# Performance work log

Measured on AMD Instinct MI355X. Metric: run time of the kernel, lower is better.

The kernel has to match this reference:

```python
import jax, jax.numpy as jnp
import numpy as np

EPS_NORM = 1e-12   # F.normalize eps
EPS_SCALE = 1e-5   # activation scale clamp


def _weight_quant(w):
    # ternary (sign) quantization with mean-abs scale
    scale = jnp.mean(jnp.abs(w))
    u = jnp.sign(w - jnp.mean(w))
    return u, scale


def _activation_quant(x):
    # SimpleRMSNorm: l2-normalize over last dim, times dim**-0.5
    dim_scale = x.shape[-1] ** -0.5
    l2 = jnp.linalg.norm(x, axis=-1, keepdims=True)
    xn = x / jnp.maximum(l2, EPS_NORM) * dim_scale
    # per-token int8 scale
    scale = 127.0 / jnp.maximum(jnp.max(jnp.abs(xn), axis=-1, keepdims=True), EPS_SCALE)
    y = jnp.clip(jnp.round(xn * scale), -128.0, 127.0)
    return y, scale


def setup_inputs() -> dict:
    key = jax.random.key(0)
    kx, kw, kb = jax.random.split(key, 3)
    B, S, D, O = 4, 8192, 1024, 1024
    x = jax.random.normal(kx, (B, S, D), dtype=jnp.float32)
    w = jax.random.normal(kw, (O, D), dtype=jnp.float32)
    b = jax.random.normal(kb, (O,), dtype=jnp.float32)
    return {"x": x, "w": w, "b": b}


def reference(x, w, b):
    w_q, w_scale = _weight_quant(w)          # [O,D], scalar
    b_q, b_scale = _weight_quant(b)          # [O], scalar
    x_q, x_scale = _activation_quant(x)      # [B,S,D], [B,S,1]
    # mm + broadcast bias add, then dequant by product of all three scales
    y = jnp.einsum('bsd,od->bso', x_q, w_q) + b_q
    return y / (w_scale * x_scale * b_scale)
```

## Files before the change

### kernel.cpp

```cpp
#include <hip/hip_runtime.h>
#include <cstdint>
#include <cstddef>


typedef __attribute__((ext_vector_type(4))) int int4v;

static constexpr int DIM = 1024;
static constexpr int OUTF = 1024;
static constexpr int MROWS = 32768;
static constexpr float INV_WN = 1.0f / (1024.0f * 1024.0f);
static constexpr float INV_BN = 1.0f / 1024.0f;

#define OFF_XSCALE 1024
#define OFF_WQ 132096
#define OFF_XQ 1180672

__device__ inline float wave_sum(float v) {
#pragma unroll
  for (int off = 32; off; off >>= 1) v += __shfl_xor(v, off);
  return v;
}
__device__ inline float wave_max(float v) {
#pragma unroll
  for (int off = 32; off; off >>= 1) v = fmaxf(v, __shfl_xor(v, off));
  return v;
}

__global__ __launch_bounds__(256) void reduce_wb(const float* __restrict__ w,
                                                 const float* __restrict__ b,
                                                 float* __restrict__ red) {
  __shared__ float ss[4], sa[4];
  const int t = threadIdx.x;
  const int lane = t & 63, wv = t >> 6;
  float s = 0.0f, a = 0.0f;
  const float4* w4 = (const float4*)w;
  const int idx = blockIdx.x * 256 + t;
#pragma unroll
  for (int i = 0; i < 4; ++i) {
    float4 v = w4[idx + i * 65536];
    s += (v.x + v.y) + (v.z + v.w);
    a += (fabsf(v.x) + fabsf(v.y)) + (fabsf(v.z) + fabsf(v.w));
  }
  s = wave_sum(s);
  a = wave_sum(a);
  if (lane == 0) { ss[wv] = s; sa[wv] = a; }
  __syncthreads();
  if (t == 0) atomicAdd(&red[0], (ss[0] + ss[1]) + (ss[2] + ss[3]));
  if (t == 1) atomicAdd(&red[1], (sa[0] + sa[1]) + (sa[2] + sa[3]));
  if (blockIdx.x == 0) {
    __syncthreads();
    float4 v = ((const float4*)b)[t];
    float s2 = (v.x + v.y) + (v.z + v.w);
    float a2 = (fabsf(v.x) + fabsf(v.y)) + (fabsf(v.z) + fabsf(v.w));
    s2 = wave_sum(s2);
    a2 = wave_max(a2) * 0.0f + wave_sum(a2);
    if (lane == 0) { ss[wv] = s2; sa[wv] = a2; }
    __syncthreads();
    if (t == 0) {
      red[2] = (ss[0] + ss[1]) + (ss[2] + ss[3]);
      red[3] = (sa[0] + sa[1]) + (sa[2] + sa[3]);
    }
  }
}

__global__ __launch_bounds__(256) void quant_w(const float* __restrict__ w,
                                               const float* __restrict__ red,
                                               signed char* __restrict__ wq) {
  const float wmean = red[0] * INV_WN;
  const int idx = blockIdx.x * 256 + threadIdx.x;
  float4 v = ((const float4*)w)[idx];
  int q0, q1, q2, q3;
  float d;
  d = v.x - wmean; q0 = d > 0.f ? 1 : (d < 0.f ? -1 : 0);
  d = v.y - wmean; q1 = d > 0.f ? 1 : (d < 0.f ? -1 : 0);
  d = v.z - wmean; q2 = d > 0.f ? 1 : (d < 0.f ? -1 : 0);
  d = v.w - wmean; q3 = d > 0.f ? 1 : (d < 0.f ? -1 : 0);
  const int pk = (q0 & 0xff) | ((q1 & 0xff) << 8) | ((q2 & 0xff) << 16) | ((q3 & 0xff) << 24);
  ((int*)wq)[idx] = pk;
}

__global__ __launch_bounds__(256) void quant_x(const float* __restrict__ x,
                                               signed char* __restrict__ xq,
                                               float* __restrict__ xscale) {
  const int wv = threadIdx.x >> 6;
  const int lane = threadIdx.x & 63;
  const int row = blockIdx.x * 4 + wv;
  const float4* xr = (const float4*)(x + (size_t)row * DIM);
  float4 v[4];
  float ss = 0.0f, ma = 0.0f;
#pragma unroll
  for (int it = 0; it < 4; ++it) {
    v[it] = xr[it * 64 + lane];
    ss += v[it].x * v[it].x + v[it].y * v[it].y + v[it].z * v[it].z + v[it].w * v[it].w;
    ma = fmaxf(ma, fmaxf(fmaxf(fabsf(v[it].x), fabsf(v[it].y)),
                         fmaxf(fabsf(v[it].z), fabsf(v[it].w))));
  }
  ss = wave_sum(ss);
  ma = wave_max(ma);

  const float l2 = sqrtf(ss);
  const float inv = 0.03125f / fmaxf(l2, 1e-12f);
  const float scale = 127.0f / fmaxf(ma * inv, 1e-5f);
  const float f = inv * scale;

  int* outp = (int*)(xq + (size_t)row * DIM);
#pragma unroll
  for (int it = 0; it < 4; ++it) {
    const int q0 = (int)fminf(fmaxf(rintf(v[it].x * f), -128.f), 127.f);
    const int q1 = (int)fminf(fmaxf(rintf(v[it].y * f), -128.f), 127.f);
    const int q2 = (int)fminf(fmaxf(rintf(v[it].z * f), -128.f), 127.f);
    const int q3 = (int)fminf(fmaxf(rintf(v[it].w * f), -128.f), 127.f);
    outp[it * 64 + lane] =
        (q0 & 0xff) | ((q1 & 0xff) << 8) | ((q2 & 0xff) << 16) | ((q3 & 0xff) << 24);
  }
  if (lane == 0) xscale[row] = scale;
}

#define BM 128
#define BN 128
#define BKB 128

__global__ __launch_bounds__(256) void gemm_i8(
    const signed char* __restrict__ Aq,
    const signed char* __restrict__ Wq,
    const float* __restrict__ bias,
    const float* __restrict__ red,
    const float* __restrict__ xscale,
    float* __restrict__ out) {
  __shared__ signed char As[BM * BKB];
  __shared__ signed char Bs[BN * BKB];

  const int t = threadIdx.x;
  const int lane = t & 63;
  const int wv = t >> 6;
  const int quad = lane >> 4;
  const int r16 = lane & 15;
  const int wm = (wv >> 1) * 64;
  const int wn = (wv & 1) * 64;
  const int bm = blockIdx.y;
  const int bn = blockIdx.x;

  int4v acc[4][4] = {};

  const char* Ab = (const char*)(Aq + (size_t)bm * BM * DIM);
  const char* Bb = (const char*)(Wq + (size_t)bn * BN * DIM);

  const int srow = lane >> 3;
  const int sbyte = (lane & 7) * 16;

  for (int k0 = 0; k0 < DIM; k0 += BKB) {
#pragma unroll
    for (int i = 0; i < 4; ++i) {
      const int c = wv * 4 + i;
      const int row = c * 8 + srow;
      __builtin_amdgcn_global_load_lds(
          (const __attribute__((address_space(1))) void*)(Ab + (size_t)row * DIM + k0 + sbyte),
          (__attribute__((address_space(3))) void*)((char*)As + c * 1024 + lane * 16),
          16, 0, 0);
      __builtin_amdgcn_global_load_lds(
          (const __attribute__((address_space(1))) void*)(Bb + (size_t)row * DIM + k0 + sbyte),
          (__attribute__((address_space(3))) void*)((char*)Bs + c * 1024 + lane * 16),
          16, 0, 0);
    }
    __syncthreads();
#pragma unroll
    for (int s = 0; s < 2; ++s) {
      int4v af[4], bf[4];
#pragma unroll
      for (int i = 0; i < 4; ++i) {
        af[i] = *(const int4v*)(As + (wm + i * 16 + r16) * BKB + s * 64 + quad * 16);
        bf[i] = *(const int4v*)(Bs + (wn + i * 16 + r16) * BKB + s * 64 + quad * 16);
      }
#pragma unroll
      for (int i = 0; i < 4; ++i)
#pragma unroll
        for (int j = 0; j < 4; ++j)
          acc[i][j] = __builtin_amdgcn_mfma_i32_16x16x64_i8(af[i], bf[j], acc[i][j], 0, 0, 0);
    }
    __syncthreads();
  }

  const float wscale = red[1] * INV_WN;
  const float bscale = red[3] * INV_BN;
  const float bmean = red[2] * INV_BN;
  const float wb = wscale * bscale;

  float rec[4][4];
#pragma unroll
  for (int i = 0; i < 4; ++i)
#pragma unroll
    for (int rr = 0; rr < 4; ++rr) {
      const int m = bm * BM + wm + i * 16 + quad * 4 + rr;
      rec[i][rr] = 1.0f / (wb * xscale[m]);
    }

#pragma unroll
  for (int j = 0; j < 4; ++j) {
    const int n = bn * BN + wn + j * 16 + r16;
    const float bd = bias[n] - bmean;
    const int bq = bd > 0.f ? 1 : (bd < 0.f ? -1 : 0);
#pragma unroll
    for (int i = 0; i < 4; ++i) {
      const int mg = bm * BM + wm + i * 16 + quad * 4;
      float* po = out + (size_t)mg * OUTF + n;
#pragma unroll
      for (int rr = 0; rr < 4; ++rr)
        po[(size_t)rr * OUTF] = (float)(acc[i][j][rr] + bq) * rec[i][rr];
    }
  }
}

extern "C" void kernel_launch(void* const* d_in, const int* in_sizes, int n_in,
                              void* d_out, int out_size, void* d_ws, size_t ws_size,
                              hipStream_t stream) {
  const float* x = (const float*)d_in[0];
  const float* w = (const float*)d_in[1];
  const float* b = (const float*)d_in[2];
  float* out = (float*)d_out;
  char* ws = (char*)d_ws;

  float* red = (float*)ws;
  float* xscale = (float*)(ws + OFF_XSCALE);
  signed char* wq = (signed char*)(ws + OFF_WQ);
  signed char* xq = (signed char*)(ws + OFF_XQ);

  hipMemsetAsync(red, 0, 4 * sizeof(float), stream);
  reduce_wb<<<256, 256, 0, stream>>>(w, b, red);
  quant_w<<<1024, 256, 0, stream>>>(w, red, wq);
  quant_x<<<MROWS / 4, 256, 0, stream>>>(x, xq, xscale);
  gemm_i8<<<dim3(OUTF / BN, MROWS / BM), 256, 0, stream>>>(xq, wq, b, red, xscale, out);
}
```

Before: 296.7 us.

## Fuse activation quantization into GEMM with full-K LDS-resident A tile

```diff
diff --git a/kernel.cpp b/kernel.cpp
--- a/kernel.cpp
+++ b/kernel.cpp
@@ -11,9 +11,8 @@
 static constexpr float INV_WN = 1.0f / (1024.0f * 1024.0f);
 static constexpr float INV_BN = 1.0f / 1024.0f;
 
-#define OFF_XSCALE 1024
-#define OFF_WQ 132096
-#define OFF_XQ 1180672
+#define OFF_WQ 1024
+#define SP 1040
 
 __device__ inline float wave_sum(float v) {
 #pragma unroll
@@ -53,7 +52,7 @@
     float s2 = (v.x + v.y) + (v.z + v.w);
     float a2 = (fabsf(v.x) + fabsf(v.y)) + (fabsf(v.z) + fabsf(v.w));
     s2 = wave_sum(s2);
-    a2 = wave_max(a2) * 0.0f + wave_sum(a2);
+    a2 = wave_sum(a2);
     if (lane == 0) { ss[wv] = s2; sa[wv] = a2; }
     __syncthreads();
     if (t == 0) {
@@ -79,133 +78,116 @@
   ((int*)wq)[idx] = pk;
 }
 
-__global__ __launch_bounds__(256) void quant_x(const float* __restrict__ x,
-                                               signed char* __restrict__ xq,
-                                               float* __restrict__ xscale) {
-  const int wv = threadIdx.x >> 6;
-  const int lane = threadIdx.x & 63;
-  const int row = blockIdx.x * 4 + wv;
-  const float4* xr = (const float4*)(x + (size_t)row * DIM);
-  float4 v[4];
-  float ss = 0.0f, ma = 0.0f;
-#pragma unroll
-  for (int it = 0; it < 4; ++it) {
-    v[it] = xr[it * 64 + lane];
-    ss += v[it].x * v[it].x + v[it].y * v[it].y + v[it].z * v[it].z + v[it].w * v[it].w;
-    ma = fmaxf(ma, fmaxf(fmaxf(fabsf(v[it].x), fabsf(v[it].y)),
-                         fmaxf(fabsf(v[it].z), fabsf(v[it].w))));
-  }
-  ss = wave_sum(ss);
-  ma = wave_max(ma);
-
-  const float l2 = sqrtf(ss);
-  const float inv = 0.03125f / fmaxf(l2, 1e-12f);
-  const float scale = 127.0f / fmaxf(ma * inv, 1e-5f);
-  const float f = inv * scale;
-
-  int* outp = (int*)(xq + (size_t)row * DIM);
-#pragma unroll
-  for (int it = 0; it < 4; ++it) {
-    const int q0 = (int)fminf(fmaxf(rintf(v[it].x * f), -128.f), 127.f);
-    const int q1 = (int)fminf(fmaxf(rintf(v[it].y * f), -128.f), 127.f);
-    const int q2 = (int)fminf(fmaxf(rintf(v[it].z * f), -128.f), 127.f);
-    const int q3 = (int)fminf(fmaxf(rintf(v[it].w * f), -128.f), 127.f);
-    outp[it * 64 + lane] =
-        (q0 & 0xff) | ((q1 & 0xff) << 8) | ((q2 & 0xff) << 16) | ((q3 & 0xff) << 24);
-  }
-  if (lane == 0) xscale[row] = scale;
-}
-
-#define BM 128
-#define BN 128
-#define BKB 128
-
-__global__ __launch_bounds__(256) void gemm_i8(
-    const signed char* __restrict__ Aq,
-    const signed char* __restrict__ Wq,
+__global__ __launch_bounds__(512, 1) void fused_qx_gemm(
+    const float* __restrict__ x,
+    const signed char* __restrict__ wq,
     const float* __restrict__ bias,
     const float* __restrict__ red,
-    const float* __restrict__ xscale,
     float* __restrict__ out) {
-  __shared__ signed char As[BM * BKB];
-  __shared__ signed char Bs[BN * BKB];
+  __shared__ signed char As[128 * SP];
+  __shared__ float sxs[128];
 
   const int t = threadIdx.x;
   const int lane = t & 63;
   const int wv = t >> 6;
   const int quad = lane >> 4;
   const int r16 = lane & 15;
-  const int wm = (wv >> 1) * 64;
-  const int wn = (wv & 1) * 64;
-  const int bm = blockIdx.y;
-  const int bn = blockIdx.x;
-
-  int4v acc[4][4] = {};
-
-  const char* Ab = (const char*)(Aq + (size_t)bm * BM * DIM);
-  const char* Bb = (const char*)(Wq + (size_t)bn * BN * DIM);
-
-  const int srow = lane >> 3;
-  const int sbyte = (lane & 7) * 16;
-
-  for (int k0 = 0; k0 < DIM; k0 += BKB) {
-#pragma unroll
-    for (int i = 0; i < 4; ++i) {
-      const int c = wv * 4 + i;
-      const int row = c * 8 + srow;
-      __builtin_amdgcn_global_load_lds(
-          (const __attribute__((address_space(1))) void*)(Ab + (size_t)row * DIM + k0 + sbyte),
-          (__attribute__((address_space(3))) void*)((char*)As + c * 1024 + lane * 16),
-          16, 0, 0);
-      __builtin_amdgcn_global_load_lds(
-          (const __attribute__((address_space(1))) void*)(Bb + (size_t)row * DIM + k0 + sbyte),
-          (__attribute__((address_space(3))) void*)((char*)Bs + c * 1024 + lane * 16),
-          16, 0, 0);
-    }
-    __syncthreads();
-#pragma unroll
-    for (int s = 0; s < 2; ++s) {
-      int4v af[4], bf[4];
-#pragma unroll
-      for (int i = 0; i < 4; ++i) {
-        af[i] = *(const int4v*)(As + (wm + i * 16 + r16) * BKB + s * 64 + quad * 16);
-        bf[i] = *(const int4v*)(Bs + (wn + i * 16 + r16) * BKB + s * 64 + quad * 16);
-      }
-#pragma unroll
-      for (int i = 0; i < 4; ++i)
-#pragma unroll
-        for (int j = 0; j < 4; ++j)
-          acc[i][j] = __builtin_amdgcn_mfma_i32_16x16x64_i8(af[i], bf[j], acc[i][j], 0, 0, 0);
-    }
-    __syncthreads();
-  }
+  const int bm = blockIdx.x;
+
+  {
+    const int row0 = wv * 16;
+    const float* xbase = x + ((size_t)bm * 128 + row0) * DIM;
+    float4 v[4], vn[4];
+#pragma unroll
+    for (int j = 0; j < 4; ++j) v[j] = ((const float4*)xbase)[j * 64 + lane];
+
+    for (int rr = 0; rr < 16; ++rr) {
+      if (rr < 15) {
+        const float4* xn = (const float4*)(xbase + (size_t)(rr + 1) * DIM);
+#pragma unroll
+        for (int j = 0; j < 4; ++j) vn[j] = xn[j * 64 + lane];
+      }
+      float ssq = 0.0f, ma = 0.0f;
+#pragma unroll
+      for (int j = 0; j < 4; ++j) {
+        ssq += v[j].x * v[j].x + v[j].y * v[j].y + v[j].z * v[j].z + v[j].w * v[j].w;
+        ma = fmaxf(ma, fmaxf(fmaxf(fabsf(v[j].x), fabsf(v[j].y)),
+                             fmaxf(fabsf(v[j].z), fabsf(v[j].w))));
+      }
+      ssq = wave_sum(ssq);
+      ma = wave_max(ma);
+
+      const float l2 = sqrtf(ssq);
+      const float inv = 0.03125f / fmaxf(l2, 1e-12f);
+      const float scale = 127.0f / fmaxf(ma * inv, 1e-5f);
+      const float f = inv * scale;
+
+      const int rl = row0 + rr;
+#pragma unroll
+      for (int j = 0; j < 4; ++j) {
+        const int q0 = (int)fminf(fmaxf(rintf(v[j].x * f), -128.f), 127.f);
+        const int q1 = (int)fminf(fmaxf(rintf(v[j].y * f), -128.f), 127.f);
+        const int q2 = (int)fminf(fmaxf(rintf(v[j].z * f), -128.f), 127.f);
+        const int q3 = (int)fminf(fmaxf(rintf(v[j].w * f), -128.f), 127.f);
+        *(int*)(As + rl * SP + j * 256 + lane * 4) =
+            (q0 & 0xff) | ((q1 & 0xff) << 8) | ((q2 & 0xff) << 16) | ((q3 & 0xff) << 24);
+      }
+      if (lane == 0) sxs[rl] = scale;
+#pragma unroll
+      for (int j = 0; j < 4; ++j) v[j] = vn[j];
+    }
+  }
+  __syncthreads();
 
   const float wscale = red[1] * INV_WN;
   const float bscale = red[3] * INV_BN;
   const float bmean = red[2] * INV_BN;
   const float wb = wscale * bscale;
 
+  const int wm2 = wv >> 2;
+  const int wn2 = wv & 3;
+
   float rec[4][4];
 #pragma unroll
   for (int i = 0; i < 4; ++i)
 #pragma unroll
-    for (int rr = 0; rr < 4; ++rr) {
-      const int m = bm * BM + wm + i * 16 + quad * 4 + rr;
-      rec[i][rr] = 1.0f / (wb * xscale[m]);
-    }
-
-#pragma unroll
-  for (int j = 0; j < 4; ++j) {
-    const int n = bn * BN + wn + j * 16 + r16;
-    const float bd = bias[n] - bmean;
-    const int bq = bd > 0.f ? 1 : (bd < 0.f ? -1 : 0);
-#pragma unroll
-    for (int i = 0; i < 4; ++i) {
-      const int mg = bm * BM + wm + i * 16 + quad * 4;
-      float* po = out + (size_t)mg * OUTF + n;
-#pragma unroll
-      for (int rr = 0; rr < 4; ++rr)
-        po[(size_t)rr * OUTF] = (float)(acc[i][j][rr] + bq) * rec[i][rr];
+    for (int rr = 0; rr < 4; ++rr)
+      rec[i][rr] = 1.0f / (wb * sxs[wm2 * 64 + i * 16 + quad * 4 + rr]);
+
+  const signed char* AsW = As + (wm2 * 64 + r16) * SP + quad * 16;
+
+  for (int nc = 0; nc < 8; ++nc) {
+    int4v acc[4][2] = {};
+    const signed char* Bb =
+        wq + ((size_t)(nc * 128 + wn2 * 32 + r16)) * DIM + quad * 16;
+#pragma unroll 4
+    for (int ks = 0; ks < 16; ++ks) {
+      int4v af[4], bf[2];
+#pragma unroll
+      for (int i = 0; i < 4; ++i)
+        af[i] = *(const int4v*)(AsW + i * 16 * SP + ks * 64);
+#pragma unroll
+      for (int j = 0; j < 2; ++j)
+        bf[j] = *(const int4v*)(Bb + (size_t)j * 16 * DIM + ks * 64);
+#pragma unroll
+      for (int i = 0; i < 4; ++i)
+#pragma unroll
+        for (int j = 0; j < 2; ++j)
+          acc[i][j] = __builtin_amdgcn_mfma_i32_16x16x64_i8(af[i], bf[j], acc[i][j], 0, 0, 0);
+    }
+#pragma unroll
+    for (int j = 0; j < 2; ++j) {
+      const int n = nc * 128 + wn2 * 32 + j * 16 + r16;
+      const float bd = bias[n] - bmean;
+      const int bq = bd > 0.f ? 1 : (bd < 0.f ? -1 : 0);
+#pragma unroll
+      for (int i = 0; i < 4; ++i) {
+        const int mg = bm * 128 + wm2 * 64 + i * 16 + quad * 4;
+        float* po = out + (size_t)mg * OUTF + n;
+#pragma unroll
+        for (int rr = 0; rr < 4; ++rr)
+          po[(size_t)rr * OUTF] = (float)(acc[i][j][rr] + bq) * rec[i][rr];
+      }
     }
   }
 }
@@ -220,13 +202,10 @@
   char* ws = (char*)d_ws;
 
   float* red = (float*)ws;
-  float* xscale = (float*)(ws + OFF_XSCALE);
   signed char* wq = (signed char*)(ws + OFF_WQ);
-  signed char* xq = (signed char*)(ws + OFF_XQ);
 
   hipMemsetAsync(red, 0, 4 * sizeof(float), stream);
   reduce_wb<<<256, 256, 0, stream>>>(w, b, red);
   quant_w<<<1024, 256, 0, stream>>>(w, red, wq);
-  quant_x<<<MROWS / 4, 256, 0, stream>>>(x, xq, xscale);
-  gemm_i8<<<dim3(OUTF / BN, MROWS / BM), 256, 0, stream>>>(xq, wq, b, red, xscale, out);
-}
+  fused_qx_gemm<<<MROWS / 128, 512, 0, stream>>>(x, wq, b, red, out);
+}
```

Measured after the change: 313.1 us. 1.06x slower.
